# Performance work log

Measured on AMD Instinct MI355X. Metric: run time of the kernel, lower is better.

Reference implementation:

```python
import jax, jax.numpy as jnp
import numpy as np


def _unpack_int4(packed):
    """Unpack int8 [O, K//2] -> fp16 [O, K]; each byte holds (high, low) signed nibbles."""
    # Arithmetic right shift on int8 reproduces torch's signed high-nibble extraction.
    high = packed >> 4                                  # [-8, 7]
    low = (packed & jnp.int8(15)).astype(jnp.int8)      # [0, 15]
    low = (low - jnp.int8(16) * (low > 7).astype(jnp.int8)).astype(jnp.int8)
    u = jnp.stack([high, low], axis=-1)                 # [O, K//2, 2]
    u = u.reshape(packed.shape[:-1] + (-1,))            # [O, K]
    return u.astype(jnp.float16)


def setup_inputs() -> dict:
    key = jax.random.key(0)
    k1, k2, k3 = jax.random.split(key, 3)
    B, S, K, O = 4, 2048, 4096, 4096
    x = jax.random.normal(k1, (B, S, K), dtype=jnp.float16)
    weight_int4 = jax.random.randint(k2, (O, K // 2), -128, 128, dtype=jnp.int32).astype(jnp.int8)
    weight_scale = jnp.asarray(0.05, dtype=jnp.float16)  # max_abs/7 style per-tensor scale
    bias = (jax.random.normal(k3, (O,), dtype=jnp.float16) * jnp.float16(0.01))
    return {"x": x, "weight_int4": weight_int4, "weight_scale": weight_scale, "bias": bias}


def reference(x, weight_int4, weight_scale, bias):
    # quantized-path forward: dequantize packed INT4 weights, then F.linear
    W = _unpack_int4(weight_int4) * weight_scale        # [O, K] fp16
    out = jnp.einsum('bsk,ok->bso', x, W)               # [B, S, O]
    return out + bias
```

## Files before the change

kernel.cpp:

```cpp
#include <hip/hip_runtime.h>
#include <hip/hip_bf16.h>
#include <stdint.h>


typedef __bf16 bf16;
typedef __bf16 bf16x8 __attribute__((ext_vector_type(8)));
typedef float  f32x4  __attribute__((ext_vector_type(4)));

constexpr int M_DIM = 8192;
constexpr int N_DIM = 4096;
constexpr int K_DIM = 4096;
constexpr int KB    = K_DIM / 2;

constexpr int BM = 128;
constexpr int BN = 128;
constexpr int BK = 64;

__device__ __forceinline__ void gload_lds16(const void* g, void* l) {
  __builtin_amdgcn_global_load_lds(
      (const __attribute__((address_space(1))) void*)g,
      (__attribute__((address_space(3))) void*)l,
      16, 0, 0);
}

__device__ __forceinline__ float dq_hi_f(int b) {
  int sb = (int)(signed char)(b & 0xFF);
  return (float)(sb >> 4);
}
__device__ __forceinline__ float dq_lo_f(int b) {
  int sb = (int)(signed char)(b & 0xFF);
  return (float)(((sb & 15) ^ 8) - 8);
}

__global__ void convert_x(const float* __restrict__ x, bf16* __restrict__ xc) {
  const size_t i = (size_t)blockIdx.x * 256 + threadIdx.x;
  const float4 a = ((const float4*)x)[2 * i];
  const float4 b = ((const float4*)x)[2 * i + 1];
  bf16x8 o;
  o[0] = (bf16)a.x; o[1] = (bf16)a.y; o[2] = (bf16)a.z; o[3] = (bf16)a.w;
  o[4] = (bf16)b.x; o[5] = (bf16)b.y; o[6] = (bf16)b.z; o[7] = (bf16)b.w;
  *(bf16x8*)(xc + i * 8) = o;
}

__global__ void dequant_w(const int* __restrict__ wq, bf16* __restrict__ W,
                          const float* __restrict__ scale_p) {
  const float s = scale_p[0];
  const size_t idx = (size_t)blockIdx.x * 256 + threadIdx.x;
  const int4 v = ((const int4*)wq)[idx];
  bf16x8 o;
  o[0] = (bf16)(dq_hi_f(v.x) * s); o[1] = (bf16)(dq_lo_f(v.x) * s);
  o[2] = (bf16)(dq_hi_f(v.y) * s); o[3] = (bf16)(dq_lo_f(v.y) * s);
  o[4] = (bf16)(dq_hi_f(v.z) * s); o[5] = (bf16)(dq_lo_f(v.z) * s);
  o[6] = (bf16)(dq_hi_f(v.w) * s); o[7] = (bf16)(dq_lo_f(v.w) * s);
  *(bf16x8*)(W + idx * 8) = o;
}

template <int MODE>
__global__ void __launch_bounds__(256)
gemm_bt(const float* __restrict__ Xf, const bf16* __restrict__ Xc,
        const bf16* __restrict__ W,  const int* __restrict__ WQ,
        const float* __restrict__ scale_p, const float* __restrict__ bias,
        float* __restrict__ out) {
  __shared__ __align__(16) bf16 As[BM][BK];
  __shared__ __align__(16) bf16 Bs[BN][BK];

  const int tid = threadIdx.x;
  const int w   = tid >> 6;
  const int l   = tid & 63;

  const int nwg = gridDim.x;
  const int cpx = nwg >> 3;
  const int bid = blockIdx.x;
  const int wg  = (bid & 7) * cpx + (bid >> 3);

  const int ntN = N_DIM / BN;
  const int m0  = (wg / ntN) * BM;
  const int n0  = (wg % ntN) * BN;

  const int wm = w >> 1, wn = w & 1;
  const int lrow = l & 15, lg = l >> 4;

  f32x4 acc[4][4] = {};

  const float s = (MODE == 2) ? scale_p[0] : 0.0f;

  const int arow = (w << 3) + (l >> 3);
  const int acol = (l & 7) << 3;
  const int rr = tid >> 1, rh = tid & 1;

  for (int k0 = 0; k0 < K_DIM; k0 += BK) {
    if constexpr (MODE == 0) {
      const bf16* gA = Xc + (size_t)(m0 + arow) * K_DIM + (k0 + acol);
#pragma unroll
      for (int i = 0; i < 4; ++i)
        gload_lds16(gA + (size_t)(i * 32) * K_DIM, &As[i * 32 + (w << 3)][0]);
    } else {
      const float* gx = Xf + (size_t)(m0 + rr) * K_DIM + k0 + rh * 32;
      float4 xa[8];
#pragma unroll
      for (int u = 0; u < 8; ++u) xa[u] = ((const float4*)gx)[u];
      bf16* dst = &As[rr][rh * 32];
#pragma unroll
      for (int u = 0; u < 4; ++u) {
        const float4 p = xa[2 * u], q = xa[2 * u + 1];
        bf16x8 o;
        o[0] = (bf16)p.x; o[1] = (bf16)p.y; o[2] = (bf16)p.z; o[3] = (bf16)p.w;
        o[4] = (bf16)q.x; o[5] = (bf16)q.y; o[6] = (bf16)q.z; o[7] = (bf16)q.w;
        *(bf16x8*)(dst + u * 8) = o;
      }
    }

    if constexpr (MODE <= 1) {
      const bf16* gB = W + (size_t)(n0 + arow) * K_DIM + (k0 + acol);
#pragma unroll
      for (int i = 0; i < 4; ++i)
        gload_lds16(gB + (size_t)(i * 32) * K_DIM, &Bs[i * 32 + (w << 3)][0]);
    } else {
      const int4* gq = (const int4*)(WQ + (size_t)(n0 + rr) * KB + (k0 >> 1) + rh * 16);
      const int4 q0 = gq[0], q1 = gq[1], q2 = gq[2], q3 = gq[3];
      const int vals[16] = {q0.x, q0.y, q0.z, q0.w, q1.x, q1.y, q1.z, q1.w,
                            q2.x, q2.y, q2.z, q2.w, q3.x, q3.y, q3.z, q3.w};
      bf16* dst = &Bs[rr][rh * 32];
#pragma unroll
      for (int u = 0; u < 4; ++u) {
        bf16x8 ov;
#pragma unroll
        for (int e = 0; e < 4; ++e) {
          const int b = vals[u * 4 + e];
          ov[e * 2]     = (bf16)(dq_hi_f(b) * s);
          ov[e * 2 + 1] = (bf16)(dq_lo_f(b) * s);
        }
        *(bf16x8*)(dst + u * 8) = ov;
      }
    }

    __syncthreads();

#pragma unroll
    for (int kk = 0; kk < BK; kk += 32) {
      bf16x8 af[4], bfr[4];
#pragma unroll
      for (int i = 0; i < 4; ++i)
        af[i] = *(const bf16x8*)&As[wm * 64 + i * 16 + lrow][kk + lg * 8];
#pragma unroll
      for (int j = 0; j < 4; ++j)
        bfr[j] = *(const bf16x8*)&Bs[wn * 64 + j * 16 + lrow][kk + lg * 8];
#pragma unroll
      for (int i = 0; i < 4; ++i)
#pragma unroll
        for (int j = 0; j < 4; ++j)
          acc[i][j] = __builtin_amdgcn_mfma_f32_16x16x32_bf16(af[i], bfr[j],
                                                              acc[i][j], 0, 0, 0);
    }

    __syncthreads();
  }

  float bv[4];
#pragma unroll
  for (int j = 0; j < 4; ++j)
    bv[j] = bias[n0 + wn * 64 + j * 16 + lrow];

#pragma unroll
  for (int i = 0; i < 4; ++i) {
#pragma unroll
    for (int r = 0; r < 4; ++r) {
      const size_t grow = (size_t)m0 + wm * 64 + i * 16 + lg * 4 + r;
      float* orow = out + grow * N_DIM + (n0 + wn * 64 + lrow);
#pragma unroll
      for (int j = 0; j < 4; ++j)
        orow[j * 16] = acc[i][j][r] + bv[j];
    }
  }
}

extern "C" void kernel_launch(void* const* d_in, const int* in_sizes, int n_in,
                              void* d_out, int out_size, void* d_ws, size_t ws_size,
                              hipStream_t stream) {
  const float* x     = (const float*)d_in[0];
  const int*   wq    = (const int*)d_in[1];
  const float* scale = (const float*)d_in[2];
  const float* bias  = (const float*)d_in[3];
  float*       out   = (float*)d_out;

  const size_t wb = (size_t)N_DIM * K_DIM * sizeof(bf16);
  const size_t xb = (size_t)M_DIM * K_DIM * sizeof(bf16);
  bf16* Wd = (bf16*)d_ws;
  bf16* Xc = (bf16*)((char*)d_ws + wb);

  const dim3 grid((M_DIM / BM) * (N_DIM / BN));

  if (ws_size >= wb + xb) {
    dequant_w<<<(N_DIM * KB / 4) / 256, 256, 0, stream>>>(wq, Wd, scale);
    convert_x<<<((size_t)M_DIM * K_DIM / 8) / 256, 256, 0, stream>>>(x, Xc);
    gemm_bt<0><<<grid, 256, 0, stream>>>(nullptr, Xc, Wd, nullptr, scale, bias, out);
  } else if (ws_size >= wb) {
    dequant_w<<<(N_DIM * KB / 4) / 256, 256, 0, stream>>>(wq, Wd, scale);
    gemm_bt<1><<<grid, 256, 0, stream>>>(x, nullptr, Wd, nullptr, scale, bias, out);
  } else {
    gemm_bt<2><<<grid, 256, 0, stream>>>(x, nullptr, nullptr, wq, scale, bias, out);
  }
}
```

Before: 569.9 us.

## Replace GEMM with 256x256 double-buffered 8-wave pipelined kernel with swizzled LDS

Replaces the 128x128 single-buffered GEMM with a 256x256 tile kernel using 512 threads, double-buffered LDS, XOR-swizzled LDS layout, and interleaved global-to-LDS loads between MFMA phases with s_setprio. It aims to raise arithmetic intensity, hide global load latency and cut LDS bank conflicts. It relies on manual vmcnt waits and barriers, so correctness depends on the counts being right. The intermediate-workspace fallback path is dropped.

```diff
diff --git a/kernel.cpp b/kernel.cpp
--- a/kernel.cpp
+++ b/kernel.cpp
@@ -12,15 +12,22 @@
 constexpr int K_DIM = 4096;
 constexpr int KB    = K_DIM / 2;
 
-constexpr int BM = 128;
-constexpr int BN = 128;
+constexpr int BM = 256;
+constexpr int BN = 256;
 constexpr int BK = 64;
+constexpr int NKT = K_DIM / BK;
 
 __device__ __forceinline__ void gload_lds16(const void* g, void* l) {
   __builtin_amdgcn_global_load_lds(
       (const __attribute__((address_space(1))) void*)g,
       (__attribute__((address_space(3))) void*)l,
       16, 0, 0);
+}
+
+__device__ __forceinline__ void fence_barrier() {
+  asm volatile("" ::: "memory");
+  __builtin_amdgcn_s_barrier();
+  asm volatile("" ::: "memory");
 }
 
 __device__ __forceinline__ float dq_hi_f(int b) {
@@ -55,89 +62,181 @@
   *(bf16x8*)(W + idx * 8) = o;
 }
 
-template <int MODE>
-__global__ void __launch_bounds__(256)
-gemm_bt(const float* __restrict__ Xf, const bf16* __restrict__ Xc,
-        const bf16* __restrict__ W,  const int* __restrict__ WQ,
-        const float* __restrict__ scale_p, const float* __restrict__ bias,
-        float* __restrict__ out) {
-  __shared__ __align__(16) bf16 As[BM][BK];
-  __shared__ __align__(16) bf16 Bs[BN][BK];
+
+#define MMA16(AF, BF, ACCOFF)                                                  \
+  {                                                                            \
+    _Pragma("unroll") for (int i_ = 0; i_ < 4; ++i_) {                         \
+      _Pragma("unroll") for (int j_ = 0; j_ < 4; ++j_) {                       \
+        acc[(ACCOFF) + i_][j_] = __builtin_amdgcn_mfma_f32_16x16x32_bf16(      \
+            (AF)[i_], (BF)[j_], acc[(ACCOFF) + i_][j_], 0, 0, 0);              \
+      }                                                                        \
+    }                                                                          \
+  }
+
+__global__ void __launch_bounds__(512, 2)
+gemm8p(const bf16* __restrict__ Xc, const bf16* __restrict__ W,
+       const float* __restrict__ bias, float* __restrict__ out) {
+  __shared__ __align__(16) bf16 As[2][BM][BK];
+  __shared__ __align__(16) bf16 Bs[2][BN][BK];
 
   const int tid = threadIdx.x;
   const int w   = tid >> 6;
   const int l   = tid & 63;
-
-  const int nwg = gridDim.x;
-  const int cpx = nwg >> 3;
+  const int wm  = w >> 2;
+  const int wn  = w & 3;
+  const int lrow = l & 15, lg = l >> 4;
+
   const int bid = blockIdx.x;
-  const int wg  = (bid & 7) * cpx + (bid >> 3);
-
-  const int ntN = N_DIM / BN;
-  const int m0  = (wg / ntN) * BM;
-  const int n0  = (wg % ntN) * BN;
-
+  const int wg  = (bid & 7) * 64 + (bid >> 3);
+  const int m0  = (wg >> 4) * BM;
+  const int n0  = (wg & 15) * BN;
+
+  const int srow = l >> 3;
+  const int scol = ((l & 7) ^ srow) << 3;
+  const bf16* gA = Xc + (size_t)(m0 + w * 16 + srow) * K_DIM + scol;
+  const bf16* gB = W  + (size_t)(n0 + w * 16 + srow) * K_DIM + scol;
+
+  const int rsw = (lrow & 7) << 3;
+
+  f32x4 acc[8][4] = {};
+
+#define STAGE_A(KT, H)                                                         \
+  {                                                                            \
+    gload_lds16(gA + (size_t)((H) * 128) * K_DIM + (KT) * BK,                  \
+                &As[(KT) & 1][(H) * 128 + w * 16][0]);                         \
+    gload_lds16(gA + (size_t)((H) * 128 + 8) * K_DIM + (KT) * BK,              \
+                &As[(KT) & 1][(H) * 128 + w * 16 + 8][0]);                     \
+  }
+#define STAGE_B(KT, H)                                                         \
+  {                                                                            \
+    gload_lds16(gB + (size_t)((H) * 128) * K_DIM + (KT) * BK,                  \
+                &Bs[(KT) & 1][(H) * 128 + w * 16][0]);                         \
+    gload_lds16(gB + (size_t)((H) * 128 + 8) * K_DIM + (KT) * BK,              \
+                &Bs[(KT) & 1][(H) * 128 + w * 16 + 8][0]);                     \
+  }
+
+  STAGE_A(0, 0); STAGE_A(0, 1); STAGE_B(0, 0); STAGE_B(0, 1);
+  STAGE_A(1, 0); STAGE_A(1, 1);
+  asm volatile("s_waitcnt vmcnt(4)" ::: "memory");
+  fence_barrier();
+
+  for (int kt = 0; kt < NKT; ++kt) {
+    const int buf = kt & 1;
+    bf16x8 a0[8], a1[8], b0[4], b1[4];
+
+    if (kt + 1 < NKT) STAGE_B(kt + 1, 0);
+#pragma unroll
+    for (int i = 0; i < 8; ++i)
+      a0[i] = *(const bf16x8*)&As[buf][wm * 128 + i * 16 + lrow][(lg * 8) ^ rsw];
+#pragma unroll
+    for (int j = 0; j < 4; ++j)
+      b0[j] = *(const bf16x8*)&Bs[buf][wn * 64 + j * 16 + lrow][(lg * 8) ^ rsw];
+    fence_barrier();
+    asm volatile("s_waitcnt lgkmcnt(0)" ::: "memory");
+    __builtin_amdgcn_s_setprio(1);
+    MMA16(a0, b0, 0);
+    __builtin_amdgcn_s_setprio(0);
+    fence_barrier();
+
+    if (kt + 1 < NKT) STAGE_B(kt + 1, 1);
+#pragma unroll
+    for (int i = 0; i < 8; ++i)
+      a1[i] = *(const bf16x8*)&As[buf][wm * 128 + i * 16 + lrow][(32 + lg * 8) ^ rsw];
+#pragma unroll
+    for (int j = 0; j < 4; ++j)
+      b1[j] = *(const bf16x8*)&Bs[buf][wn * 64 + j * 16 + lrow][(32 + lg * 8) ^ rsw];
+    fence_barrier();
+    asm volatile("s_waitcnt lgkmcnt(0)" ::: "memory");
+    __builtin_amdgcn_s_setprio(1);
+    MMA16(a0 + 4, b0, 4);
+    __builtin_amdgcn_s_setprio(0);
+    fence_barrier();
+
+    if (kt + 2 < NKT) STAGE_A(kt + 2, 0);
+    fence_barrier();
+    __builtin_amdgcn_s_setprio(1);
+    MMA16(a1, b1, 0);
+    __builtin_amdgcn_s_setprio(0);
+    fence_barrier();
+
+    if (kt + 2 < NKT) STAGE_A(kt + 2, 1);
+    __builtin_amdgcn_s_setprio(1);
+    MMA16(a1 + 4, b1, 4);
+    __builtin_amdgcn_s_setprio(0);
+    if (kt + 2 < NKT) {
+      asm volatile("s_waitcnt vmcnt(4)" ::: "memory");
+    } else {
+      asm volatile("s_waitcnt vmcnt(0)" ::: "memory");
+    }
+    fence_barrier();
+  }
+
+  float bv[4];
+#pragma unroll
+  for (int j = 0; j < 4; ++j) bv[j] = bias[n0 + wn * 64 + j * 16 + lrow];
+
+#pragma unroll
+  for (int i = 0; i < 8; ++i) {
+#pragma unroll
+    for (int r = 0; r < 4; ++r) {
+      float* orow = out + (size_t)(m0 + wm * 128 + i * 16 + lg * 4 + r) * N_DIM
+                        + (n0 + wn * 64 + lrow);
+#pragma unroll
+      for (int j = 0; j < 4; ++j) orow[j * 16] = acc[i][j][r] + bv[j];
+    }
+  }
+}
+
+__global__ void __launch_bounds__(256)
+gemm_fused(const float* __restrict__ Xf, const int* __restrict__ WQ,
+           const float* __restrict__ scale_p, const float* __restrict__ bias,
+           float* __restrict__ out) {
+  __shared__ __align__(16) bf16 As[128][64];
+  __shared__ __align__(16) bf16 Bs[128][64];
+  const int tid = threadIdx.x;
+  const int w = tid >> 6, l = tid & 63;
+  const int nwg = gridDim.x, cpx = nwg >> 3, bid = blockIdx.x;
+  const int wg = (bid & 7) * cpx + (bid >> 3);
+  const int ntN = N_DIM / 128;
+  const int m0 = (wg / ntN) * 128, n0 = (wg % ntN) * 128;
   const int wm = w >> 1, wn = w & 1;
   const int lrow = l & 15, lg = l >> 4;
-
   f32x4 acc[4][4] = {};
-
-  const float s = (MODE == 2) ? scale_p[0] : 0.0f;
-
-  const int arow = (w << 3) + (l >> 3);
-  const int acol = (l & 7) << 3;
+  const float s = scale_p[0];
   const int rr = tid >> 1, rh = tid & 1;
-
-  for (int k0 = 0; k0 < K_DIM; k0 += BK) {
-    if constexpr (MODE == 0) {
-      const bf16* gA = Xc + (size_t)(m0 + arow) * K_DIM + (k0 + acol);
-#pragma unroll
-      for (int i = 0; i < 4; ++i)
-        gload_lds16(gA + (size_t)(i * 32) * K_DIM, &As[i * 32 + (w << 3)][0]);
-    } else {
-      const float* gx = Xf + (size_t)(m0 + rr) * K_DIM + k0 + rh * 32;
-      float4 xa[8];
-#pragma unroll
-      for (int u = 0; u < 8; ++u) xa[u] = ((const float4*)gx)[u];
-      bf16* dst = &As[rr][rh * 32];
-#pragma unroll
-      for (int u = 0; u < 4; ++u) {
-        const float4 p = xa[2 * u], q = xa[2 * u + 1];
-        bf16x8 o;
-        o[0] = (bf16)p.x; o[1] = (bf16)p.y; o[2] = (bf16)p.z; o[3] = (bf16)p.w;
-        o[4] = (bf16)q.x; o[5] = (bf16)q.y; o[6] = (bf16)q.z; o[7] = (bf16)q.w;
-        *(bf16x8*)(dst + u * 8) = o;
+  for (int k0 = 0; k0 < K_DIM; k0 += 64) {
+    const float* gx = Xf + (size_t)(m0 + rr) * K_DIM + k0 + rh * 32;
+    float4 xa[8];
+#pragma unroll
+    for (int u = 0; u < 8; ++u) xa[u] = ((const float4*)gx)[u];
+    bf16* dst = &As[rr][rh * 32];
+#pragma unroll
+    for (int u = 0; u < 4; ++u) {
+      const float4 p = xa[2 * u], q = xa[2 * u + 1];
+      bf16x8 o;
+      o[0] = (bf16)p.x; o[1] = (bf16)p.y; o[2] = (bf16)p.z; o[3] = (bf16)p.w;
+      o[4] = (bf16)q.x; o[5] = (bf16)q.y; o[6] = (bf16)q.z; o[7] = (bf16)q.w;
+      *(bf16x8*)(dst + u * 8) = o;
+    }
+    const int4* gq = (const int4*)(WQ + (size_t)(n0 + rr) * KB + (k0 >> 1) + rh * 16);
+    const int4 q0 = gq[0], q1 = gq[1], q2 = gq[2], q3 = gq[3];
+    const int vals[16] = {q0.x, q0.y, q0.z, q0.w, q1.x, q1.y, q1.z, q1.w,
+                          q2.x, q2.y, q2.z, q2.w, q3.x, q3.y, q3.z, q3.w};
+    bf16* bdst = &Bs[rr][rh * 32];
+#pragma unroll
+    for (int u = 0; u < 4; ++u) {
+      bf16x8 ov;
+#pragma unroll
+      for (int e = 0; e < 4; ++e) {
+        const int b = vals[u * 4 + e];
+        ov[e * 2]     = (bf16)(dq_hi_f(b) * s);
+        ov[e * 2 + 1] = (bf16)(dq_lo_f(b) * s);
       }
-    }
-
-    if constexpr (MODE <= 1) {
-      const bf16* gB = W + (size_t)(n0 + arow) * K_DIM + (k0 + acol);
-#pragma unroll
-      for (int i = 0; i < 4; ++i)
-        gload_lds16(gB + (size_t)(i * 32) * K_DIM, &Bs[i * 32 + (w << 3)][0]);
-    } else {
-      const int4* gq = (const int4*)(WQ + (size_t)(n0 + rr) * KB + (k0 >> 1) + rh * 16);
-      const int4 q0 = gq[0], q1 = gq[1], q2 = gq[2], q3 = gq[3];
-      const int vals[16] = {q0.x, q0.y, q0.z, q0.w, q1.x, q1.y, q1.z, q1.w,
-                            q2.x, q2.y, q2.z, q2.w, q3.x, q3.y, q3.z, q3.w};
-      bf16* dst = &Bs[rr][rh * 32];
-#pragma unroll
-      for (int u = 0; u < 4; ++u) {
-        bf16x8 ov;
-#pragma unroll
-        for (int e = 0; e < 4; ++e) {
-          const int b = vals[u * 4 + e];
-          ov[e * 2]     = (bf16)(dq_hi_f(b) * s);
-          ov[e * 2 + 1] = (bf16)(dq_lo_f(b) * s);
-        }
-        *(bf16x8*)(dst + u * 8) = ov;
-      }
-    }
-
+      *(bf16x8*)(bdst + u * 8) = ov;
+    }
     __syncthreads();
-
-#pragma unroll
-    for (int kk = 0; kk < BK; kk += 32) {
+#pragma unroll
+    for (int kk = 0; kk < 64; kk += 32) {
       bf16x8 af[4], bfr[4];
 #pragma unroll
       for (int i = 0; i < 4; ++i)
@@ -152,26 +251,20 @@
           acc[i][j] = __builtin_amdgcn_mfma_f32_16x16x32_bf16(af[i], bfr[j],
                                                               acc[i][j], 0, 0, 0);
     }
-
     __syncthreads();
   }
-
   float bv[4];
 #pragma unroll
-  for (int j = 0; j < 4; ++j)
-    bv[j] = bias[n0 + wn * 64 + j * 16 + lrow];
-
-#pragma unroll
-  for (int i = 0; i < 4; ++i) {
+  for (int j = 0; j < 4; ++j) bv[j] = bias[n0 + wn * 64 + j * 16 + lrow];
+#pragma unroll
+  for (int i = 0; i < 4; ++i)
 #pragma unroll
     for (int r = 0; r < 4; ++r) {
-      const size_t grow = (size_t)m0 + wm * 64 + i * 16 + lg * 4 + r;
-      float* orow = out + grow * N_DIM + (n0 + wn * 64 + lrow);
-#pragma unroll
-      for (int j = 0; j < 4; ++j)
-        orow[j * 16] = acc[i][j][r] + bv[j];
-    }
-  }
+      float* orow = out + (size_t)(m0 + wm * 64 + i * 16 + lg * 4 + r) * N_DIM
+                        + (n0 + wn * 64 + lrow);
+#pragma unroll
+      for (int j = 0; j < 4; ++j) orow[j * 16] = acc[i][j][r] + bv[j];
+    }
 }
 
 extern "C" void kernel_launch(void* const* d_in, const int* in_sizes, int n_in,
@@ -185,19 +278,15 @@
 
   const size_t wb = (size_t)N_DIM * K_DIM * sizeof(bf16);
   const size_t xb = (size_t)M_DIM * K_DIM * sizeof(bf16);
-  bf16* Wd = (bf16*)d_ws;
-  bf16* Xc = (bf16*)((char*)d_ws + wb);
-
-  const dim3 grid((M_DIM / BM) * (N_DIM / BN));
 
   if (ws_size >= wb + xb) {
+    bf16* Wd = (bf16*)d_ws;
+    bf16* Xc = (bf16*)((char*)d_ws + wb);
     dequant_w<<<(N_DIM * KB / 4) / 256, 256, 0, stream>>>(wq, Wd, scale);
     convert_x<<<((size_t)M_DIM * K_DIM / 8) / 256, 256, 0, stream>>>(x, Xc);
-    gemm_bt<0><<<grid, 256, 0, stream>>>(nullptr, Xc, Wd, nullptr, scale, bias, out);
-  } else if (ws_size >= wb) {
-    dequant_w<<<(N_DIM * KB / 4) / 256, 256, 0, stream>>>(wq, Wd, scale);
-    gemm_bt<1><<<grid, 256, 0, stream>>>(x, nullptr, Wd, nullptr, scale, bias, out);
+    gemm8p<<<dim3((M_DIM / BM) * (N_DIM / BN)), 512, 0, stream>>>(Xc, Wd, bias, out);
   } else {
-    gemm_bt<2><<<grid, 256, 0, stream>>>(x, nullptr, nullptr, wq, scale, bias, out);
-  }
-}
+    gemm_fused<<<dim3((M_DIM / 128) * (N_DIM / 128)), 256, 0, stream>>>(
+        x, wq, scale, bias, out);
+  }
+}
```

Measured after the change: 533.8 us. -6.3%, faster.
